# Kernel optimization log

Measured on AMD Instinct MI355X. Metric: run time of the kernel, lower is better.

## Reference

```python
import jax, jax.numpy as jnp
import numpy as np

BN_EPS = 1e-3  # keras BatchNormalization default epsilon


def conv1x1(x, w):
    # x: [N,C,H,W], w: [O,C] (1x1 conv, no bias)
    return jnp.einsum('nchw,oc->nohw', x, w)


def bn(x, gamma, beta, mean, var):
    # inference-mode batchnorm over channel axis 1
    scale = gamma / jnp.sqrt(var + BN_EPS)
    shift = beta - mean * scale
    return x * scale[None, :, None, None] + shift[None, :, None, None]


def fourier_unit(x, w, gamma, beta, mean, var):
    # x: [N,C,H,W] NCHW. 1D rfft over W (matches tf.signal.rfft), normalized by sqrt(W).
    N, C, H, W = x.shape
    norm = jnp.sqrt(jnp.float32(W))
    f = jnp.fft.rfft(x / norm, axis=-1)          # [N,C,H,Wf] complex64, Wf=W//2+1
    Wf = f.shape[-1]
    # interleave re/im per channel: [N,C,2,H,Wf] -> [N,2C,H,Wf]
    ff = jnp.stack([jnp.real(f), jnp.imag(f)], axis=2).reshape(N, 2 * C, H, Wf)
    y = jax.nn.relu(bn(conv1x1(ff, w), gamma, beta, mean, var))  # [N,2C,H,Wf]
    Co = y.shape[1] // 2
    y = y.reshape(N, Co, 2, H, Wf)
    c = jax.lax.complex(y[:, :, 0], y[:, :, 1])
    return jnp.fft.irfft(c, n=W, axis=-1) * norm  # [N,Co,H,W]


def setup_inputs() -> dict:
    key = jax.random.key(0)
    ks = jax.random.split(key, 20)
    N, H, W, Cin = 8, 128, 128, 256
    fmaps = 256
    half = fmaps // 2  # 128

    def nrm(k, shape, s=0.05):
        return jax.random.normal(k, shape, dtype=jnp.float32) * s

    def bn_params(k, c):
        k1, k2, k3, k4 = jax.random.split(k, 4)
        gamma = jax.random.uniform(k1, (c,), dtype=jnp.float32) + 0.5
        beta = nrm(k2, (c,), 0.1)
        mean = nrm(k3, (c,), 0.1)
        var = jax.random.uniform(k4, (c,), dtype=jnp.float32) + 0.5
        return gamma, beta, mean, var

    x = jax.random.normal(ks[0], (N, H, W, Cin), dtype=jnp.float32)
    w1 = nrm(ks[1], (half, Cin))
    g1, b1, m1, v1 = bn_params(ks[2], half)
    fu_w = nrm(ks[3], (2 * half, 2 * half))
    fu_g, fu_b, fu_m, fu_v = bn_params(ks[4], 2 * half)
    lfu_w = nrm(ks[5], (2 * half, 2 * half))
    lfu_g, lfu_b, lfu_m, lfu_v = bn_params(ks[6], 2 * half)
    w2 = nrm(ks[7], (fmaps, half))
    return {
        'x': x, 'w1': w1, 'g1': g1, 'b1': b1, 'm1': m1, 'v1': v1,
        'fu_w': fu_w, 'fu_g': fu_g, 'fu_b': fu_b, 'fu_m': fu_m, 'fu_v': fu_v,
        'lfu_w': lfu_w, 'lfu_g': lfu_g, 'lfu_b': lfu_b, 'lfu_m': lfu_m, 'lfu_v': lfu_v,
        'w2': w2,
    }


def reference(x, w1, g1, b1, m1, v1,
              fu_w, fu_g, fu_b, fu_m, fu_v,
              lfu_w, lfu_g, lfu_b, lfu_m, lfu_v,
              w2):
    # NHWC -> NCHW (stride=1, no downsample)
    x = jnp.transpose(x, (0, 3, 1, 2))
    x = jax.nn.relu(bn(conv1x1(x, w1), g1, b1, m1, v1))  # [N,half,H,W]
    out = fourier_unit(x, fu_w, fu_g, fu_b, fu_m, fu_v)
    # local fourier unit: take first C//4 channels, fold 2x2 spatial patches into channels
    C = x.shape[1]
    xs = x[:, :C // 4]
    xs = jnp.concatenate(jnp.split(xs, 2, axis=2), axis=1)  # split H
    xs = jnp.concatenate(jnp.split(xs, 2, axis=3), axis=1)  # split W -> [N,C,H/2,W/2]
    xs = fourier_unit(xs, lfu_w, lfu_g, lfu_b, lfu_m, lfu_v)
    xs = jnp.tile(xs, (1, 1, 2, 2))  # back to [N,C,H,W]
    out = conv1x1(x + out + xs, w2)  # [N,fmaps,H,W]
    return jnp.transpose(out, (0, 2, 3, 1))  # NCHW -> NHWC
```

## Files before the change

### kernel.cpp

```cpp
#include <hip/hip_runtime.h>
#include <math.h>

typedef __attribute__((ext_vector_type(8))) short short8;
typedef __attribute__((ext_vector_type(4))) float f32x4;

#define SW7b(r) (((r) & 7) << 4)
#define SW3b(r) (((r) & 3) << 4)

static __device__ __forceinline__ unsigned short f2b(float f){
  unsigned u = __float_as_uint(f);
  u = (u + 0x7FFFu + ((u >> 16) & 1u)) >> 16;
  return (unsigned short)u;
}
static __device__ __forceinline__ float b2f(unsigned short u){
  return __uint_as_float(((unsigned)u) << 16);
}
static __device__ __forceinline__ void gl16(const void* g, void* l) {
  __builtin_amdgcn_global_load_lds(
      (const __attribute__((address_space(1))) void*)g,
      (__attribute__((address_space(3))) void*)l, 16, 0, 0);
}

__global__ void k_wt(const float* __restrict__ w1, const float* __restrict__ fu_w,
                     const float* __restrict__ lfu_w, const float* __restrict__ w2,
                     const float* __restrict__ g1, const float* __restrict__ b1,
                     const float* __restrict__ m1, const float* __restrict__ v1,
                     const float* __restrict__ fg, const float* __restrict__ fb,
                     const float* __restrict__ fm, const float* __restrict__ fv,
                     const float* __restrict__ lg_, const float* __restrict__ lb_,
                     const float* __restrict__ lm_, const float* __restrict__ lv_,
                     unsigned short* __restrict__ w1b, unsigned short* __restrict__ fuwb,
                     unsigned short* __restrict__ lfuwb, unsigned short* __restrict__ w2b,
                     unsigned short* __restrict__ DFTf, unsigned short* __restrict__ IDFTf,
                     unsigned short* __restrict__ DFTl, unsigned short* __restrict__ IDFTl,
                     float* __restrict__ sc1, float* __restrict__ sh1,
                     float* __restrict__ scF, float* __restrict__ shF,
                     float* __restrict__ scL, float* __restrict__ shL) {
  int t = blockIdx.x * 256 + threadIdx.x;
  const float TPI = 6.283185307179586f;
  if (t < 32768) {
    { int co = t >> 8, k = t & 255; w1b[co * 256 + (k ^ ((co & 7) << 3))] = f2b(w1[t]); }
    { int co = t >> 7, k = t & 127; w2b[co * 128 + (k ^ ((co & 7) << 3))] = f2b(w2[t]); }
  }
  if (t < 65536) {
    int co = t >> 8, k = t & 255;
    fuwb[co * 256 + (k ^ ((co & 7) << 3))] = f2b(fu_w[t]);
    lfuwb[co * 256 + (k ^ ((co & 7) << 3))] = f2b(lfu_w[t]);
  }
  if (t < 18432) {
    int m = t >> 7, w = t & 127; float v = 0.f;
    if (m < 130) {
      int wf = m >> 1; int ph = (wf * w) & 127;
      float ang = TPI * (float)ph / 128.f;
      v = ((m & 1) ? -sinf(ang) : cosf(ang)) * 0.08838834764831845f;
    }
    DFTf[m * 128 + (w ^ ((m & 7) << 3))] = f2b(v);
  }
  if (t < 24576) {
    int m = t / 192, k2 = t % 192; float v = 0.f;
    if (k2 < 130) {
      int wf = k2 >> 1; float a = (wf == 0 || wf == 64) ? 1.f : 2.f;
      int ph = (wf * m) & 127;
      float ang = TPI * (float)ph / 128.f;
      v = ((k2 & 1) ? -a * sinf(ang) : a * cosf(ang)) * 0.08838834764831845f;
    }
    IDFTf[m * 192 + (k2 ^ ((m & 7) << 3))] = f2b(v);
  }
  if (t < 5120) {
    int m = t >> 6, w = t & 63; float v = 0.f;
    if (m < 66) {
      int wf = m >> 1; int ph = (wf * w) & 63;
      float ang = TPI * (float)ph / 64.f;
      v = ((m & 1) ? -sinf(ang) : cosf(ang)) * 0.125f;
    }
    DFTl[m * 64 + (w ^ ((m & 7) << 3))] = f2b(v);
  }
  if (t < 6144) {
    int m = t / 96, k2 = t % 96; float v = 0.f;
    if (k2 < 66) {
      int wf = k2 >> 1; float a = (wf == 0 || wf == 32) ? 1.f : 2.f;
      int ph = (wf * m) & 63;
      float ang = TPI * (float)ph / 64.f;
      v = ((k2 & 1) ? -a * sinf(ang) : a * cosf(ang)) * 0.125f;
    }
    IDFTl[m * 96 + (k2 ^ ((m & 3) << 3))] = f2b(v);
  }
  if (t < 128) { float s = g1[t] * rsqrtf(v1[t] + 1e-3f); sc1[t] = s; sh1[t] = b1[t] - m1[t] * s; }
  if (t < 256) { float s = fg[t] * rsqrtf(fv[t] + 1e-3f); scF[t] = s; shF[t] = fb[t] - fm[t] * s; }
  if (t < 256) { float s = lg_[t] * rsqrtf(lv_[t] + 1e-3f); scL[t] = s; shL[t] = lb_[t] - lm_[t] * s; }
}

__global__ __launch_bounds__(512) void k_conv1(const unsigned short* __restrict__ A,
                                               const float* __restrict__ x,
                                               unsigned short* __restrict__ X1c,
                                               const float* __restrict__ scp,
                                               const float* __restrict__ shp) {
  __shared__ __align__(16) char A_s[128 * 512];
  __shared__ __align__(16) char B_s[2][32768];
  int t = threadIdx.x; int wid = t >> 6, l = t & 63;
  int wm = wid >> 2, wn = wid & 3;
  int m0 = wm * 64, n0 = wn * 64;
  int lr = l & 15, lg = l >> 4;
  size_t nh0 = (size_t)blockIdx.x * 2;
  const char* Ab = (const char*)A;
  const char* xrow = (const char*)(x + nh0 * 32768);
  #pragma unroll
  for (int i = 0; i < 8; i++) { int g = i * 512 + t; gl16(Ab + g * 16, A_s + g * 16); }
  #pragma unroll
  for (int i = 0; i < 4; i++) {
    int g = i * 512 + t; int w = g >> 3, o = g & 7;
    gl16(xrow + (size_t)w * 1024 + ((o * 16) ^ SW7b(w)), B_s[0] + g * 16);
  }
  f32x4 acc[4][4];
  #pragma unroll
  for (int mt = 0; mt < 4; mt++)
    #pragma unroll
    for (int nt = 0; nt < 4; nt++) acc[mt][nt] = (f32x4){0.f, 0.f, 0.f, 0.f};
  __syncthreads();
  for (int it = 0; it < 8; it++) {
    int kk = it * 32;
    if (it < 7) {
      #pragma unroll
      for (int i = 0; i < 4; i++) {
        int g = i * 512 + t; int w = g >> 3, o = g & 7;
        gl16(xrow + (size_t)w * 1024 + (kk + 32) * 4 + ((o * 16) ^ SW7b(w)),
             B_s[(it + 1) & 1] + g * 16);
      }
    }
    const char* Bc = B_s[it & 1];
    short8 af[4], bf[4];
    #pragma unroll
    for (int mt = 0; mt < 4; mt++) {
      int m = m0 + 16 * mt + lr;
      af[mt] = *(const short8*)(A_s + m * 512 + ((kk * 2 + lg * 16) ^ SW7b(m)));
    }
    #pragma unroll
    for (int nt = 0; nt < 4; nt++) {
      int w = n0 + 16 * nt + lr;
      float4 f0 = *(const float4*)(Bc + w * 128 + ((lg * 32) ^ SW7b(w)));
      float4 f1 = *(const float4*)(Bc + w * 128 + ((lg * 32 + 16) ^ SW7b(w)));
      short8 bb;
      bb[0] = (short)f2b(f0.x); bb[1] = (short)f2b(f0.y);
      bb[2] = (short)f2b(f0.z); bb[3] = (short)f2b(f0.w);
      bb[4] = (short)f2b(f1.x); bb[5] = (short)f2b(f1.y);
      bb[6] = (short)f2b(f1.z); bb[7] = (short)f2b(f1.w);
      bf[nt] = bb;
    }
    #pragma unroll
    for (int mt = 0; mt < 4; mt++)
      #pragma unroll
      for (int nt = 0; nt < 4; nt++)
        acc[mt][nt] = __builtin_amdgcn_mfma_f32_16x16x32_bf16(af[mt], bf[nt], acc[mt][nt], 0, 0, 0);
    __syncthreads();
  }
  #pragma unroll
  for (int nt = 0; nt < 4; nt++) {
    int wcol = n0 + 16 * nt + lr;
    char* xout = (char*)X1c + (nh0 + (wcol >> 7)) * 32768;
    int w = wcol & 127;
    #pragma unroll
    for (int mt = 0; mt < 4; mt++) {
      int rb = m0 + 16 * mt + lg * 4;
      float4 s4 = *(const float4*)&scp[rb];
      float4 h4 = *(const float4*)&shp[rb];
      f32x4 v = acc[mt][nt];
      *(unsigned short*)(xout + (rb + 0) * 256 + ((w * 2) ^ SW7b(rb + 0))) = f2b(fmaxf(v[0] * s4.x + h4.x, 0.f));
      *(unsigned short*)(xout + (rb + 1) * 256 + ((w * 2) ^ SW7b(rb + 1))) = f2b(fmaxf(v[1] * s4.y + h4.y, 0.f));
      *(unsigned short*)(xout + (rb + 2) * 256 + ((w * 2) ^ SW7b(rb + 2))) = f2b(fmaxf(v[2] * s4.z + h4.z, 0.f));
      *(unsigned short*)(xout + (rb + 3) * 256 + ((w * 2) ^ SW7b(rb + 3))) = f2b(fmaxf(v[3] * s4.w + h4.w, 0.f));
    }
  }
}

__global__ __launch_bounds__(256) void k_lfu(const unsigned short* __restrict__ DFTm,
                                             const unsigned short* __restrict__ lfuw,
                                             const unsigned short* __restrict__ IDFTm,
                                             const unsigned short* __restrict__ X1c,
                                             const float* __restrict__ scp,
                                             const float* __restrict__ shp,
                                             unsigned short* __restrict__ XSO) {
  __shared__ __align__(16) char SH[81920];
  char* M   = SH;
  char* Xs  = SH + 16384;
  char* FFl = SH + 32768;
  char* Yl  = SH + 57344;
  int t = threadIdx.x, wid = t >> 6, l = t & 63, lr = l & 15, lg = l >> 4;
  int b = blockIdx.x; int n = b >> 6, h2 = b & 63;
  {
    const char* src = (const char*)DFTm;
    #pragma unroll
    for (int i = 0; i < 3; i++) { int g = i * 256 + t; if (g < 640) gl16(src + g * 16, M + g * 16); }
    #pragma unroll
    for (int i = 0; i < 4; i++) {
      int g = i * 256 + t; int c2 = g >> 3, o = g & 7;
      int c0 = c2 & 31, hb = (c2 >> 5) & 1, wbq = (c2 >> 6) & 1;
      const char* s = (const char*)X1c +
          ((size_t)(n * 128 + hb * 64 + h2) * 128 + c0) * 256 + wbq * 128 + o * 16;
      gl16(s, Xs + g * 16);
    }
    #pragma unroll
    for (int i = 0; i < 8; i++) {
      int u = i * 256 + t;
      if (u < 1920) *(unsigned*)(FFl + 33 * 512 + u * 4) = 0u;
    }
  }
  __syncthreads();
  {
    f32x4 acc[5][2];
    #pragma unroll
    for (int mt = 0; mt < 5; mt++) { acc[mt][0] = (f32x4){0,0,0,0}; acc[mt][1] = (f32x4){0,0,0,0}; }
    for (int kk = 0; kk < 64; kk += 32) {
      int kb = kk * 2 + lg * 16;
      short8 bf[2];
      #pragma unroll
      for (int nt = 0; nt < 2; nt++) {
        int c2 = wid * 32 + 16 * nt + lr;
        bf[nt] = *(const short8*)(Xs + c2 * 128 + (kb ^ SW7b(c2)));
      }
      #pragma unroll
      for (int mt = 0; mt < 5; mt++) {
        int m = 16 * mt + lr;
        short8 af = *(const short8*)(M + m * 128 + (kb ^ SW7b(m)));
        #pragma unroll
        for (int nt = 0; nt < 2; nt++)
          acc[mt][nt] = __builtin_amdgcn_mfma_f32_16x16x32_bf16(af, bf[nt], acc[mt][nt], 0, 0, 0);
      }
    }
    #pragma unroll
    for (int nt = 0; nt < 2; nt++) {
      int c2 = wid * 32 + 16 * nt + lr;
      #pragma unroll
      for (int mt = 0; mt < 5; mt++) {
        int rb = 16 * mt + lg * 4;
        int wf0 = rb >> 1;
        f32x4 v = acc[mt][nt];
        if (wf0 < 33) {
          unsigned pk = (unsigned)f2b(v[0]) | ((unsigned)f2b(v[1]) << 16);
          *(unsigned*)(FFl + wf0 * 512 + ((4 * c2) ^ SW7b(wf0))) = pk;
        }
        if (wf0 + 1 < 33) {
          unsigned pk = (unsigned)f2b(v[2]) | ((unsigned)f2b(v[3]) << 16);
          *(unsigned*)(FFl + (wf0 + 1) * 512 + ((4 * c2) ^ SW7b(wf0 + 1))) = pk;
        }
      }
    }
  }
  __syncthreads();
  int wm2 = wid >> 1, wn2 = wid & 1;
  for (int ch = 0; ch < 8; ch++) {
    {
      const char* src = (const char*)lfuw + (size_t)ch * 16384;
      #pragma unroll
      for (int i = 0; i < 4; i++) { int g = i * 256 + t; gl16(src + g * 16, M + g * 16); }
    }
    __syncthreads();
    int NT = wn2 ? 1 : 2;
    f32x4 acc[2];
    acc[0] = (f32x4){0,0,0,0}; acc[1] = (f32x4){0,0,0,0};
    int lm = wm2 * 16 + lr;
    for (int kk = 0; kk < 256; kk += 32) {
      int kb = kk * 2 + lg * 16;
      short8 af = *(const short8*)(M + lm * 512 + (kb ^ SW7b(lm)));
      #pragma unroll
      for (int j = 0; j < 2; j++) {
        if (j < NT) {
          int wf = wn2 * 32 + 16 * j + lr;
          short8 bf = *(const short8*)(FFl + wf * 512 + (kb ^ SW7b(wf)));
          acc[j] = __builtin_amdgcn_mfma_f32_16x16x32_bf16(af, bf, acc[j], 0, 0, 0);
        }
      }
    }
    int co = ch * 32 + wm2 * 16 + lg * 4;
    float4 s4 = *(const float4*)&scp[co];
    float4 h4 = *(const float4*)&shp[co];
    int cc0 = co >> 1;
    #pragma unroll
    for (int j = 0; j < 2; j++) {
      if (j < NT) {
        int wf = wn2 * 32 + 16 * j + lr;
        f32x4 v = acc[j];
        float v0 = fmaxf(v[0] * s4.x + h4.x, 0.f);
        float v1 = fmaxf(v[1] * s4.y + h4.y, 0.f);
        float v2 = fmaxf(v[2] * s4.z + h4.z, 0.f);
        float v3 = fmaxf(v[3] * s4.w + h4.w, 0.f);
        unsigned p0 = (unsigned)f2b(v0) | ((unsigned)f2b(v1) << 16);
        unsigned p1 = (unsigned)f2b(v2) | ((unsigned)f2b(v3) << 16);
        *(unsigned*)(Yl + (cc0 + 0) * 192 + ((4 * wf) ^ SW3b(cc0 + 0))) = p0;
        *(unsigned*)(Yl + (cc0 + 1) * 192 + ((4 * wf) ^ SW3b(cc0 + 1))) = p1;
      }
    }
    __syncthreads();
  }
  {
    const char* src = (const char*)IDFTm;
    #pragma unroll
    for (int i = 0; i < 3; i++) { int g = i * 256 + t; gl16(src + g * 16, M + g * 16); }
  }
  __syncthreads();
  {
    f32x4 acc[8];
    #pragma unroll
    for (int nt = 0; nt < 8; nt++) acc[nt] = (f32x4){0,0,0,0};
    int w = wid * 16 + lr;
    for (int kk = 0; kk < 96; kk += 32) {
      int kb = kk * 2 + lg * 16;
      short8 af = *(const short8*)(M + w * 192 + (kb ^ SW3b(w)));
      #pragma unroll
      for (int nt = 0; nt < 8; nt++) {
        int cc = 16 * nt + lr;
        short8 bf = *(const short8*)(Yl + cc * 192 + (kb ^ SW3b(cc)));
        acc[nt] = __builtin_amdgcn_mfma_f32_16x16x32_bf16(af, bf, acc[nt], 0, 0, 0);
      }
    }
    int w0 = wid * 16 + lg * 4;
    #pragma unroll
    for (int nt = 0; nt < 8; nt++) {
      int cc = 16 * nt + lr;
      f32x4 v = acc[nt];
      ushort4 o;
      o.x = f2b(v[0]); o.y = f2b(v[1]); o.z = f2b(v[2]); o.w = f2b(v[3]);
      *(ushort4*)(XSO + (((size_t)n * 128 + cc) * 64 + h2) * 64 + w0) = o;
    }
  }
}

__global__ __launch_bounds__(1024, 4) void k_fu(const unsigned short* __restrict__ DFTm,
                                                const unsigned short* __restrict__ fuw,
                                                const unsigned short* __restrict__ IDFTm,
                                                const unsigned short* __restrict__ w2m,
                                                const unsigned short* __restrict__ X1c,
                                                const unsigned short* __restrict__ XSO,
                                                const float* __restrict__ scF,
                                                const float* __restrict__ shF,
                                                float* __restrict__ out) {
  __shared__ __align__(16) char SH[157696];
  char* M0 = SH;
  char* M1 = SH + 36864;
  char* FF = SH + 73728;
  char* Yb = SH + 114688;
  int t = threadIdx.x, wid = t >> 6, l = t & 63, lr = l & 15, lg = l >> 4;
  size_t nh = blockIdx.x;
  int n = (int)(nh >> 7), h = (int)(nh & 127);
  const char* xb = (const char*)X1c + nh * 32768;
  char* Xs = M0 + 0;
  (void)Xs;

  {
    const int nops = 36864 >> 4;
    #pragma unroll
    for (int i_ = 0; i_ < 3; i_++) {
      int g_ = i_ * 1024 + t;
      if (g_ < nops) gl16((const char*)DFTm + (size_t)g_ * 16, M0 + g_ * 16);
    }
    if (t < 1920) *(unsigned*)(FF + 65 * 512 + t * 4) = 0u;
  }
  __syncthreads();
  {
    #pragma unroll
    for (int i_ = 0; i_ < 2; i_++) {
      int g_ = i_ * 1024 + t;
      gl16((const char*)fuw + (size_t)g_ * 16, M1 + g_ * 16);
    }
    int wm1 = wid >> 3, wn1 = wid & 7;
    int c = wn1 * 16 + lr;
    short8 bf[4];
    #pragma unroll
    for (int ks = 0; ks < 4; ks++)
      bf[ks] = *(const short8*)(xb + c * 256 + ((ks * 64 + lg * 16) ^ SW7b(c)));
    f32x4 acc[5];
    #pragma unroll
    for (int mt = 0; mt < 5; mt++) acc[mt] = (f32x4){0,0,0,0};
    #pragma unroll
    for (int ks = 0; ks < 4; ks++) {
      int kb = ks * 64 + lg * 16;
      #pragma unroll
      for (int mt = 0; mt < 5; mt++) {
        int m = 16 * (wm1 * 4 + mt) + lr;
        short8 af = *(const short8*)(M0 + m * 256 + (kb ^ SW7b(m)));
        acc[mt] = __builtin_amdgcn_mfma_f32_16x16x32_bf16(af, bf[ks], acc[mt], 0, 0, 0);
      }
    }
    #pragma unroll
    for (int mt = 0; mt < 5; mt++) {
      int rb = 16 * (wm1 * 4 + mt) + lg * 4;
      int wf0 = rb >> 1;
      f32x4 v = acc[mt];
      if (wf0 < 65) {
        unsigned pk = (unsigned)f2b(v[0]) | ((unsigned)f2b(v[1]) << 16);
        *(unsigned*)(FF + wf0 * 512 + ((4 * c) ^ SW7b(wf0))) = pk;
      }
      if (wf0 + 1 < 65) {
        unsigned pk = (unsigned)f2b(v[2]) | ((unsigned)f2b(v[3]) << 16);
        *(unsigned*)(FF + (wf0 + 1) * 512 + ((4 * c) ^ SW7b(wf0 + 1))) = pk;
      }
    }
  }
  int mb2 = wid & 3, wn2 = wid >> 2;
  int mloc2 = mb2 * 16 + lr;
  #pragma unroll
  for (int ch = 0; ch < 4; ch++) {
    char* Mc = (ch & 1) ? M0 : M1;
    char* Mn = (ch & 1) ? M1 : M0;
    __syncthreads();
    if (ch < 3) {
      #pragma unroll
      for (int i_ = 0; i_ < 2; i_++) {
        int g_ = i_ * 1024 + t;
        gl16((const char*)fuw + (size_t)(ch + 1) * 32768 + (size_t)g_ * 16, Mn + g_ * 16);
      }
    } else {
      #pragma unroll
      for (int i_ = 0; i_ < 2; i_++) {
        int g_ = i_ * 1024 + t;
        if (g_ < 1536) gl16((const char*)IDFTm + (size_t)g_ * 16, Mn + g_ * 16);
      }
    }
    f32x4 acc[2];
    acc[0] = (f32x4){0,0,0,0}; acc[1] = (f32x4){0,0,0,0};
    int NJ = (wn2 == 0) ? 2 : 1;
    int j0 = wn2, j1 = 4;
    #pragma unroll
    for (int ks = 0; ks < 8; ks++) {
      int kb = ks * 64 + lg * 16;
      short8 af = *(const short8*)(Mc + mloc2 * 512 + (kb ^ SW7b(mloc2)));
      {
        int wf = j0 * 16 + lr;
        short8 b0 = *(const short8*)(FF + wf * 512 + (kb ^ SW7b(wf)));
        acc[0] = __builtin_amdgcn_mfma_f32_16x16x32_bf16(af, b0, acc[0], 0, 0, 0);
      }
      if (NJ == 2) {
        int wf = j1 * 16 + lr;
        short8 b1 = *(const short8*)(FF + wf * 512 + (kb ^ SW7b(wf)));
        acc[1] = __builtin_amdgcn_mfma_f32_16x16x32_bf16(af, b1, acc[1], 0, 0, 0);
      }
    }
    int co = ch * 64 + mb2 * 16 + lg * 4;
    float4 s4 = *(const float4*)&scF[co];
    float4 h4 = *(const float4*)&shF[co];
    int cc0 = co >> 1;
    #pragma unroll
    for (int jj = 0; jj < 2; jj++) {
      if (jj < NJ) {
        int wf = (jj == 0 ? j0 : j1) * 16 + lr;
        f32x4 v = acc[jj];
        float v0 = fmaxf(v[0] * s4.x + h4.x, 0.f);
        float v1 = fmaxf(v[1] * s4.y + h4.y, 0.f);
        float v2 = fmaxf(v[2] * s4.z + h4.z, 0.f);
        float v3 = fmaxf(v[3] * s4.w + h4.w, 0.f);
        unsigned p0 = (unsigned)f2b(v0) | ((unsigned)f2b(v1) << 16);
        unsigned p1 = (unsigned)f2b(v2) | ((unsigned)f2b(v3) << 16);
        *(unsigned*)(Yb + (size_t)(cc0 + 0) * 336 + 4 * wf) = p0;
        *(unsigned*)(Yb + (size_t)(cc0 + 1) * 336 + 4 * wf) = p1;
      }
    }
  }
  int mb3 = wid & 3, wn3 = wid >> 2;
  #pragma unroll
  for (int ck = 0; ck < 2; ck++) {
    char* Mc = ck ? M0 : M1;
    __syncthreads();
    if (ck == 0) {
      #pragma unroll
      for (int i_ = 0; i_ < 2; i_++) {
        int g_ = i_ * 1024 + t;
        if (g_ < 1536) gl16((const char*)IDFTm + 24576 + (size_t)g_ * 16, M0 + g_ * 16);
      }
    } else {
      #pragma unroll
      for (int i_ = 0; i_ < 2; i_++) {
        int g_ = i_ * 1024 + t;
        gl16((const char*)w2m + (size_t)g_ * 16, M1 + g_ * 16);
      }
    }
    int mloc = mb3 * 16 + lr;
    int w0 = ck * 64 + mb3 * 16 + lg * 4;
    ushort4 rx[2], rs[2];
    #pragma unroll
    for (int jj = 0; jj < 2; jj++) {
      int cc = (wn3 + jj * 4) * 16 + lr;
      rx[jj] = *(const ushort4*)(xb + cc * 256 + ((w0 * 2) ^ SW7b(cc)));
      rs[jj] = *(const ushort4*)(XSO + (((size_t)n * 128 + cc) * 64 + (h & 63)) * 64 + (w0 & 63));
    }
    f32x4 acc[2];
    acc[0] = (f32x4){0,0,0,0}; acc[1] = (f32x4){0,0,0,0};
    #pragma unroll
    for (int ks = 0; ks < 5; ks++) {
      int kb = ks * 64 + lg * 16;
      short8 af = *(const short8*)(Mc + mloc * 384 + (kb ^ SW7b(mloc)));
      #pragma unroll
      for (int jj = 0; jj < 2; jj++) {
        int cc = (wn3 + jj * 4) * 16 + lr;
        short8 bf = *(const short8*)(Yb + (size_t)cc * 336 + kb);
        acc[jj] = __builtin_amdgcn_mfma_f32_16x16x32_bf16(af, bf, acc[jj], 0, 0, 0);
      }
    }
    #pragma unroll
    for (int jj = 0; jj < 2; jj++) {
      int cc = (wn3 + jj * 4) * 16 + lr;
      f32x4 v = acc[jj];
      float f0 = v[0] + b2f(rx[jj].x) + b2f(rs[jj].x);
      float f1 = v[1] + b2f(rx[jj].y) + b2f(rs[jj].y);
      float f2_ = v[2] + b2f(rx[jj].z) + b2f(rs[jj].z);
      float f3 = v[3] + b2f(rx[jj].w) + b2f(rs[jj].w);
      *(unsigned short*)(FF + (w0 + 0) * 256 + ((cc * 2) ^ SW7b(w0 + 0))) = f2b(f0);
      *(unsigned short*)(FF + (w0 + 1) * 256 + ((cc * 2) ^ SW7b(w0 + 1))) = f2b(f1);
      *(unsigned short*)(FF + (w0 + 2) * 256 + ((cc * 2) ^ SW7b(w0 + 2))) = f2b(f2_);
      *(unsigned short*)(FF + (w0 + 3) * 256 + ((cc * 2) ^ SW7b(w0 + 3))) = f2b(f3);
    }
  }
  int mb4 = wid & 7, wn4 = wid >> 3;
  int mloc4 = mb4 * 16 + lr;
  #pragma unroll
  for (int ck = 0; ck < 2; ck++) {
    char* Mc = ck ? M0 : M1;
    __syncthreads();
    if (ck == 0) {
      #pragma unroll
      for (int i_ = 0; i_ < 2; i_++) {
        int g_ = i_ * 1024 + t;
        gl16((const char*)w2m + 32768 + (size_t)g_ * 16, M0 + g_ * 16);
      }
    }
    f32x4 acc[4];
    #pragma unroll
    for (int nt = 0; nt < 4; nt++) acc[nt] = (f32x4){0,0,0,0};
    #pragma unroll
    for (int ks = 0; ks < 4; ks++) {
      int kb = ks * 64 + lg * 16;
      short8 af = *(const short8*)(Mc + mloc4 * 256 + (kb ^ SW7b(mloc4)));
      #pragma unroll
      for (int nt = 0; nt < 4; nt++) {
        int w = (wn4 * 4 + nt) * 16 + lr;
        short8 bf = *(const short8*)(FF + w * 256 + (kb ^ SW7b(w)));
        acc[nt] = __builtin_amdgcn_mfma_f32_16x16x32_bf16(af, bf, acc[nt], 0, 0, 0);
      }
    }
    int co2 = ck * 128 + mb4 * 16 + lg * 4;
    #pragma unroll
    for (int nt = 0; nt < 4; nt++) {
      int w = (wn4 * 4 + nt) * 16 + lr;
      f32x4 v = acc[nt];
      float4 o; o.x = v[0]; o.y = v[1]; o.z = v[2]; o.w = v[3];
      *(float4*)(out + (nh * 128 + w) * 256 + co2) = o;
    }
  }
}

extern "C" void kernel_launch(void* const* d_in, const int* in_sizes, int n_in,
                              void* d_out, int out_size, void* d_ws, size_t ws_size,
                              hipStream_t stream) {
  const float* x     = (const float*)d_in[0];
  const float* w1    = (const float*)d_in[1];
  const float* g1    = (const float*)d_in[2];
  const float* b1    = (const float*)d_in[3];
  const float* m1    = (const float*)d_in[4];
  const float* v1    = (const float*)d_in[5];
  const float* fu_w  = (const float*)d_in[6];
  const float* fu_g  = (const float*)d_in[7];
  const float* fu_b  = (const float*)d_in[8];
  const float* fu_m  = (const float*)d_in[9];
  const float* fu_v  = (const float*)d_in[10];
  const float* lfu_w = (const float*)d_in[11];
  const float* lfu_g = (const float*)d_in[12];
  const float* lfu_b = (const float*)d_in[13];
  const float* lfu_m = (const float*)d_in[14];
  const float* lfu_v = (const float*)d_in[15];
  const float* w2    = (const float*)d_in[16];
  float* out = (float*)d_out;

  char* p = (char*)d_ws;
  unsigned short* X1c = (unsigned short*)p; p += 33554432;
  unsigned short* XSO = (unsigned short*)p; p += 8388608;
  unsigned short* w1b   = (unsigned short*)p; p += 65536;
  unsigned short* fuwb  = (unsigned short*)p; p += 131072;
  unsigned short* lfuwb = (unsigned short*)p; p += 131072;
  unsigned short* w2b   = (unsigned short*)p; p += 65536;
  unsigned short* DFTf  = (unsigned short*)p; p += 36864;
  unsigned short* IDFTf = (unsigned short*)p; p += 49152;
  unsigned short* DFTl  = (unsigned short*)p; p += 10240;
  unsigned short* IDFTl = (unsigned short*)p; p += 12288;
  float* sc1 = (float*)p; p += 512;
  float* sh1 = (float*)p; p += 512;
  float* scF = (float*)p; p += 1024;
  float* shF = (float*)p; p += 1024;
  float* scL = (float*)p; p += 1024;
  float* shL = (float*)p; p += 1024;

  k_wt<<<dim3(256), dim3(256), 0, stream>>>(w1, fu_w, lfu_w, w2, g1, b1, m1, v1,
                                            fu_g, fu_b, fu_m, fu_v, lfu_g, lfu_b, lfu_m, lfu_v,
                                            w1b, fuwb, lfuwb, w2b, DFTf, IDFTf, DFTl, IDFTl,
                                            sc1, sh1, scF, shF, scL, shL);
  k_conv1<<<dim3(512), dim3(512), 0, stream>>>(w1b, x, X1c, sc1, sh1);
  k_lfu<<<dim3(512), dim3(256), 0, stream>>>(DFTl, lfuwb, IDFTl, X1c, scL, shL, XSO);
  k_fu<<<dim3(1024), dim3(1024), 0, stream>>>(DFTf, fuwb, IDFTf, w2b, X1c, XSO, scF, shF, out);
}
```

Baseline: 152.3 us.

## Rewrite k_fu stages with 32x32x16 MFMA tiles and wider LDS swizzles

The fused Fourier-unit kernel moves from 16x16x32 MFMA tiles to 32x32x16 tiles in all four GEMM stages (DFT, spectral 1x1 conv, inverse DFT, output conv). Weight and DFT matrix layouts change to a 16-row XOR swizzle and a K-chunked fu_w layout to match, and the DFT table is padded. The inverse DFT now runs as a single pass over all 128 outputs instead of two chunks, which removes barriers. The intent is fewer LDS fragment loads per MFMA and fewer synchronisation points, at the cost of more accumulator registers and a slightly larger LDS footprint.

```diff
diff --git a/kernel.cpp b/kernel.cpp
--- a/kernel.cpp
+++ b/kernel.cpp
@@ -3,9 +3,12 @@
 
 typedef __attribute__((ext_vector_type(8))) short short8;
 typedef __attribute__((ext_vector_type(4))) float f32x4;
+typedef __attribute__((ext_vector_type(16))) float f32x16;
 
 #define SW7b(r) (((r) & 7) << 4)
 #define SW3b(r) (((r) & 3) << 4)
+#define K15(r) (((r) & 15) << 4)
+#define K7(r)  (((r) & 7) << 4)
 
 static __device__ __forceinline__ unsigned short f2b(float f){
   unsigned u = __float_as_uint(f);
@@ -40,21 +43,21 @@
   const float TPI = 6.283185307179586f;
   if (t < 32768) {
     { int co = t >> 8, k = t & 255; w1b[co * 256 + (k ^ ((co & 7) << 3))] = f2b(w1[t]); }
-    { int co = t >> 7, k = t & 127; w2b[co * 128 + (k ^ ((co & 7) << 3))] = f2b(w2[t]); }
+    { int co = t >> 7, k = t & 127; w2b[co * 128 + (k ^ ((co & 15) << 3))] = f2b(w2[t]); }
   }
   if (t < 65536) {
     int co = t >> 8, k = t & 255;
-    fuwb[co * 256 + (k ^ ((co & 7) << 3))] = f2b(fu_w[t]);
+    fuwb[(size_t)(k >> 6) * 16384 + co * 64 + ((k & 63) ^ ((co & 7) << 3))] = f2b(fu_w[t]);
     lfuwb[co * 256 + (k ^ ((co & 7) << 3))] = f2b(lfu_w[t]);
   }
-  if (t < 18432) {
+  if (t < 20480) {
     int m = t >> 7, w = t & 127; float v = 0.f;
     if (m < 130) {
       int wf = m >> 1; int ph = (wf * w) & 127;
       float ang = TPI * (float)ph / 128.f;
       v = ((m & 1) ? -sinf(ang) : cosf(ang)) * 0.08838834764831845f;
     }
-    DFTf[m * 128 + (w ^ ((m & 7) << 3))] = f2b(v);
+    DFTf[m * 128 + (w ^ ((m & 15) << 3))] = f2b(v);
   }
   if (t < 24576) {
     int m = t / 192, k2 = t % 192; float v = 0.f;
@@ -164,10 +167,10 @@
       float4 s4 = *(const float4*)&scp[rb];
       float4 h4 = *(const float4*)&shp[rb];
       f32x4 v = acc[mt][nt];
-      *(unsigned short*)(xout + (rb + 0) * 256 + ((w * 2) ^ SW7b(rb + 0))) = f2b(fmaxf(v[0] * s4.x + h4.x, 0.f));
-      *(unsigned short*)(xout + (rb + 1) * 256 + ((w * 2) ^ SW7b(rb + 1))) = f2b(fmaxf(v[1] * s4.y + h4.y, 0.f));
-      *(unsigned short*)(xout + (rb + 2) * 256 + ((w * 2) ^ SW7b(rb + 2))) = f2b(fmaxf(v[2] * s4.z + h4.z, 0.f));
-      *(unsigned short*)(xout + (rb + 3) * 256 + ((w * 2) ^ SW7b(rb + 3))) = f2b(fmaxf(v[3] * s4.w + h4.w, 0.f));
+      *(unsigned short*)(xout + (rb + 0) * 256 + ((w * 2) ^ K15(rb + 0))) = f2b(fmaxf(v[0] * s4.x + h4.x, 0.f));
+      *(unsigned short*)(xout + (rb + 1) * 256 + ((w * 2) ^ K15(rb + 1))) = f2b(fmaxf(v[1] * s4.y + h4.y, 0.f));
+      *(unsigned short*)(xout + (rb + 2) * 256 + ((w * 2) ^ K15(rb + 2))) = f2b(fmaxf(v[2] * s4.z + h4.z, 0.f));
+      *(unsigned short*)(xout + (rb + 3) * 256 + ((w * 2) ^ K15(rb + 3))) = f2b(fmaxf(v[3] * s4.w + h4.w, 0.f));
     }
   }
 }
@@ -194,8 +197,9 @@
     for (int i = 0; i < 4; i++) {
       int g = i * 256 + t; int c2 = g >> 3, o = g & 7;
       int c0 = c2 & 31, hb = (c2 >> 5) & 1, wbq = (c2 >> 6) & 1;
+      int half = wbq ^ ((c0 >> 3) & 1);
       const char* s = (const char*)X1c +
-          ((size_t)(n * 128 + hb * 64 + h2) * 128 + c0) * 256 + wbq * 128 + o * 16;
+          ((size_t)(n * 128 + hb * 64 + h2) * 128 + c0) * 256 + half * 128 + o * 16;
       gl16(s, Xs + g * 16);
     }
     #pragma unroll
@@ -333,215 +337,206 @@
                                                 const float* __restrict__ scF,
                                                 const float* __restrict__ shF,
                                                 float* __restrict__ out) {
-  __shared__ __align__(16) char SH[157696];
-  char* M0 = SH;
-  char* M1 = SH + 36864;
-  char* FF = SH + 73728;
-  char* Yb = SH + 114688;
-  int t = threadIdx.x, wid = t >> 6, l = t & 63, lr = l & 15, lg = l >> 4;
+  __shared__ __align__(16) char SH[161792];
+  char* R0 = SH;
+  char* R1 = SH + 40960;
+  char* R2 = SH + 73728;
+  char* R3 = SH + 122880;
+  int t = threadIdx.x, wid = t >> 6, l = t & 63;
+  int lc = l & 31, hf = l >> 5;
   size_t nh = blockIdx.x;
-  int n = (int)(nh >> 7), h = (int)(nh & 127);
+  int n = (int)(nh >> 7), hh = (int)(nh & 127);
   const char* xb = (const char*)X1c + nh * 32768;
-  char* Xs = M0 + 0;
-  (void)Xs;
-
-  {
-    const int nops = 36864 >> 4;
-    #pragma unroll
-    for (int i_ = 0; i_ < 3; i_++) {
-      int g_ = i_ * 1024 + t;
-      if (g_ < nops) gl16((const char*)DFTm + (size_t)g_ * 16, M0 + g_ * 16);
-    }
-    if (t < 1920) *(unsigned*)(FF + 65 * 512 + t * 4) = 0u;
-  }
-  __syncthreads();
-  {
-    #pragma unroll
-    for (int i_ = 0; i_ < 2; i_++) {
-      int g_ = i_ * 1024 + t;
-      gl16((const char*)fuw + (size_t)g_ * 16, M1 + g_ * 16);
-    }
-    int wm1 = wid >> 3, wn1 = wid & 7;
-    int c = wn1 * 16 + lr;
-    short8 bf[4];
-    #pragma unroll
-    for (int ks = 0; ks < 4; ks++)
-      bf[ks] = *(const short8*)(xb + c * 256 + ((ks * 64 + lg * 16) ^ SW7b(c)));
-    f32x4 acc[5];
-    #pragma unroll
-    for (int mt = 0; mt < 5; mt++) acc[mt] = (f32x4){0,0,0,0};
-    #pragma unroll
-    for (int ks = 0; ks < 4; ks++) {
-      int kb = ks * 64 + lg * 16;
-      #pragma unroll
-      for (int mt = 0; mt < 5; mt++) {
-        int m = 16 * (wm1 * 4 + mt) + lr;
-        short8 af = *(const short8*)(M0 + m * 256 + (kb ^ SW7b(m)));
-        acc[mt] = __builtin_amdgcn_mfma_f32_16x16x32_bf16(af, bf[ks], acc[mt], 0, 0, 0);
-      }
-    }
-    #pragma unroll
-    for (int mt = 0; mt < 5; mt++) {
-      int rb = 16 * (wm1 * 4 + mt) + lg * 4;
-      int wf0 = rb >> 1;
-      f32x4 v = acc[mt];
-      if (wf0 < 65) {
-        unsigned pk = (unsigned)f2b(v[0]) | ((unsigned)f2b(v[1]) << 16);
-        *(unsigned*)(FF + wf0 * 512 + ((4 * c) ^ SW7b(wf0))) = pk;
-      }
-      if (wf0 + 1 < 65) {
-        unsigned pk = (unsigned)f2b(v[2]) | ((unsigned)f2b(v[3]) << 16);
-        *(unsigned*)(FF + (wf0 + 1) * 512 + ((4 * c) ^ SW7b(wf0 + 1))) = pk;
-      }
-    }
-  }
-  int mb2 = wid & 3, wn2 = wid >> 2;
-  int mloc2 = mb2 * 16 + lr;
-  #pragma unroll
-  for (int ch = 0; ch < 4; ch++) {
-    char* Mc = (ch & 1) ? M0 : M1;
-    char* Mn = (ch & 1) ? M1 : M0;
-    __syncthreads();
-    if (ch < 3) {
-      #pragma unroll
-      for (int i_ = 0; i_ < 2; i_++) {
-        int g_ = i_ * 1024 + t;
-        gl16((const char*)fuw + (size_t)(ch + 1) * 32768 + (size_t)g_ * 16, Mn + g_ * 16);
-      }
-    } else {
-      #pragma unroll
-      for (int i_ = 0; i_ < 2; i_++) {
-        int g_ = i_ * 1024 + t;
-        if (g_ < 1536) gl16((const char*)IDFTm + (size_t)g_ * 16, Mn + g_ * 16);
-      }
-    }
-    f32x4 acc[2];
-    acc[0] = (f32x4){0,0,0,0}; acc[1] = (f32x4){0,0,0,0};
-    int NJ = (wn2 == 0) ? 2 : 1;
-    int j0 = wn2, j1 = 4;
+
+  #pragma unroll
+  for (int i = 0; i < 3; i++) {
+    int g = i * 1024 + t;
+    if (g < 2560) gl16((const char*)DFTm + (size_t)g * 16, R0 + g * 16);
+  }
+  *(unsigned*)(R2 + 80 * 512 + t * 8) = 0u;
+  *(unsigned*)(R2 + 80 * 512 + t * 8 + 4) = 0u;
+  __syncthreads();
+  {
+    #pragma unroll
+    for (int i = 0; i < 2; i++) {
+      int g = i * 1024 + t;
+      gl16((const char*)fuw + (size_t)g * 16, R1 + g * 16);
+    }
+    int mb = wid & 3, nb = wid >> 2;
+    int c = nb * 32 + lc;
+    short8 bfp[8];
+    #pragma unroll
+    for (int ks = 0; ks < 8; ks++)
+      bfp[ks] = *(const short8*)(xb + (size_t)c * 256 + ((ks * 32 + hf * 16) ^ K15(c)));
+    f32x16 acc0 = {0}, acc1 = {0};
+    bool x2 = (wid < 4);
+    int c2b = wid * 32 + lc;
     #pragma unroll
     for (int ks = 0; ks < 8; ks++) {
-      int kb = ks * 64 + lg * 16;
-      short8 af = *(const short8*)(Mc + mloc2 * 512 + (kb ^ SW7b(mloc2)));
+      int ko = ks * 32 + hf * 16;
+      int m = mb * 32 + lc;
+      short8 af = *(const short8*)(R0 + (size_t)m * 256 + (ko ^ K15(m)));
+      acc0 = __builtin_amdgcn_mfma_f32_32x32x16_bf16(af, bfp[ks], acc0, 0, 0, 0);
+      if (x2) {
+        int m2 = 128 + lc;
+        short8 af2 = *(const short8*)(R0 + (size_t)m2 * 256 + (ko ^ K15(m2)));
+        short8 bf2 = *(const short8*)(xb + (size_t)c2b * 256 + (ko ^ K15(c2b)));
+        acc1 = __builtin_amdgcn_mfma_f32_32x32x16_bf16(af2, bf2, acc1, 0, 0, 0);
+      }
+    }
+    #pragma unroll
+    for (int q = 0; q < 4; q++) {
+      int wfe = mb * 16 + 4 * q + 2 * hf;
+      unsigned p0 = (unsigned)f2b(acc0[4 * q + 0]) | ((unsigned)f2b(acc0[4 * q + 1]) << 16);
+      unsigned p1 = (unsigned)f2b(acc0[4 * q + 2]) | ((unsigned)f2b(acc0[4 * q + 3]) << 16);
+      *(unsigned*)(R2 + (size_t)wfe * 512 + ((4 * c) ^ K15(wfe))) = p0;
+      *(unsigned*)(R2 + (size_t)(wfe + 1) * 512 + ((4 * c) ^ K15(wfe + 1))) = p1;
+    }
+    if (x2) {
+      #pragma unroll
+      for (int q = 0; q < 4; q++) {
+        int wfe = 64 + 4 * q + 2 * hf;
+        unsigned p0 = (unsigned)f2b(acc1[4 * q + 0]) | ((unsigned)f2b(acc1[4 * q + 1]) << 16);
+        unsigned p1 = (unsigned)f2b(acc1[4 * q + 2]) | ((unsigned)f2b(acc1[4 * q + 3]) << 16);
+        *(unsigned*)(R2 + (size_t)wfe * 512 + ((4 * c2b) ^ K15(wfe))) = p0;
+        *(unsigned*)(R2 + (size_t)(wfe + 1) * 512 + ((4 * c2b) ^ K15(wfe + 1))) = p1;
+      }
+    }
+  }
+  {
+    int mb = wid >> 1, odd = wid & 1;
+    int co = mb * 32 + lc;
+    f32x16 pa = {0}, pb = {0};
+    int wfA = (odd ? 32 : 0) + lc;
+    int wfB = 64 + lc;
+    #pragma unroll
+    for (int ch = 0; ch < 4; ch++) {
+      char* Mc = (ch & 1) ? R0 : R1;
+      char* Mn = (ch & 1) ? R1 : R0;
+      __syncthreads();
+      if (ch < 3) {
+        #pragma unroll
+        for (int i = 0; i < 2; i++) {
+          int g = i * 1024 + t;
+          gl16((const char*)fuw + (size_t)(ch + 1) * 32768 + (size_t)g * 16, Mn + g * 16);
+        }
+      } else {
+        #pragma unroll
+        for (int i = 0; i < 2; i++) {
+          int g = i * 1024 + t;
+          gl16((const char*)w2m + (size_t)g * 16, Mn + g * 16);
+        }
+      }
+      #pragma unroll
+      for (int ks = 0; ks < 4; ks++) {
+        int ko = ks * 32 + hf * 16;
+        short8 af = *(const short8*)(Mc + (size_t)co * 128 + (ko ^ K7(co)));
+        int kg = (ch * 4 + ks) * 32 + hf * 16;
+        short8 bfA = *(const short8*)(R2 + (size_t)wfA * 512 + (kg ^ K15(wfA)));
+        pa = __builtin_amdgcn_mfma_f32_32x32x16_bf16(af, bfA, pa, 0, 0, 0);
+        if (!odd) {
+          short8 bfB = *(const short8*)(R2 + (size_t)wfB * 512 + (kg ^ K15(wfB)));
+          pb = __builtin_amdgcn_mfma_f32_32x32x16_bf16(af, bfB, pb, 0, 0, 0);
+        }
+      }
+    }
+    #pragma unroll
+    for (int q = 0; q < 4; q++) {
+      int co0 = mb * 32 + 8 * q + 4 * hf;
+      float4 s4 = *(const float4*)&scF[co0];
+      float4 h4 = *(const float4*)&shF[co0];
+      int cc0 = co0 >> 1;
       {
-        int wf = j0 * 16 + lr;
-        short8 b0 = *(const short8*)(FF + wf * 512 + (kb ^ SW7b(wf)));
-        acc[0] = __builtin_amdgcn_mfma_f32_16x16x32_bf16(af, b0, acc[0], 0, 0, 0);
-      }
-      if (NJ == 2) {
-        int wf = j1 * 16 + lr;
-        short8 b1 = *(const short8*)(FF + wf * 512 + (kb ^ SW7b(wf)));
-        acc[1] = __builtin_amdgcn_mfma_f32_16x16x32_bf16(af, b1, acc[1], 0, 0, 0);
-      }
-    }
-    int co = ch * 64 + mb2 * 16 + lg * 4;
-    float4 s4 = *(const float4*)&scF[co];
-    float4 h4 = *(const float4*)&shF[co];
-    int cc0 = co >> 1;
-    #pragma unroll
-    for (int jj = 0; jj < 2; jj++) {
-      if (jj < NJ) {
-        int wf = (jj == 0 ? j0 : j1) * 16 + lr;
-        f32x4 v = acc[jj];
-        float v0 = fmaxf(v[0] * s4.x + h4.x, 0.f);
-        float v1 = fmaxf(v[1] * s4.y + h4.y, 0.f);
-        float v2 = fmaxf(v[2] * s4.z + h4.z, 0.f);
-        float v3 = fmaxf(v[3] * s4.w + h4.w, 0.f);
+        float v0 = fmaxf(pa[4 * q + 0] * s4.x + h4.x, 0.f);
+        float v1 = fmaxf(pa[4 * q + 1] * s4.y + h4.y, 0.f);
+        float v2 = fmaxf(pa[4 * q + 2] * s4.z + h4.z, 0.f);
+        float v3 = fmaxf(pa[4 * q + 3] * s4.w + h4.w, 0.f);
         unsigned p0 = (unsigned)f2b(v0) | ((unsigned)f2b(v1) << 16);
         unsigned p1 = (unsigned)f2b(v2) | ((unsigned)f2b(v3) << 16);
-        *(unsigned*)(Yb + (size_t)(cc0 + 0) * 336 + 4 * wf) = p0;
-        *(unsigned*)(Yb + (size_t)(cc0 + 1) * 336 + 4 * wf) = p1;
-      }
-    }
-  }
-  int mb3 = wid & 3, wn3 = wid >> 2;
-  #pragma unroll
-  for (int ck = 0; ck < 2; ck++) {
-    char* Mc = ck ? M0 : M1;
+        *(unsigned*)(R3 + (size_t)(cc0 + 0) * 304 + 4 * wfA) = p0;
+        *(unsigned*)(R3 + (size_t)(cc0 + 1) * 304 + 4 * wfA) = p1;
+      }
+      if (!odd && lc < 12) {
+        float v0 = fmaxf(pb[4 * q + 0] * s4.x + h4.x, 0.f);
+        float v1 = fmaxf(pb[4 * q + 1] * s4.y + h4.y, 0.f);
+        float v2 = fmaxf(pb[4 * q + 2] * s4.z + h4.z, 0.f);
+        float v3 = fmaxf(pb[4 * q + 3] * s4.w + h4.w, 0.f);
+        unsigned p0 = (unsigned)f2b(v0) | ((unsigned)f2b(v1) << 16);
+        unsigned p1 = (unsigned)f2b(v2) | ((unsigned)f2b(v3) << 16);
+        *(unsigned*)(R3 + (size_t)(cc0 + 0) * 304 + 4 * wfB) = p0;
+        *(unsigned*)(R3 + (size_t)(cc0 + 1) * 304 + 4 * wfB) = p1;
+      }
+    }
+  }
+  __syncthreads();
+  #pragma unroll
+  for (int i = 0; i < 3; i++) {
+    int g = i * 1024 + t;
+    gl16((const char*)IDFTm + (size_t)g * 16, R2 + g * 16);
+  }
+  #pragma unroll
+  for (int i = 0; i < 2; i++) {
+    int g = i * 1024 + t;
+    gl16((const char*)w2m + 32768 + (size_t)g * 16, R0 + g * 16);
+  }
+  __syncthreads();
+  {
+    int mb = wid & 3, nb = wid >> 2;
+    int mw = mb * 32 + lc;
+    int cc = nb * 32 + lc;
+    f32x16 p3 = {0};
+    #pragma unroll
+    for (int ks = 0; ks < 9; ks++) {
+      int ko = ks * 32 + hf * 16;
+      short8 af = *(const short8*)(R2 + (size_t)mw * 384 + (ko ^ K7(mw)));
+      short8 bf = *(const short8*)(R3 + (size_t)cc * 304 + ko);
+      p3 = __builtin_amdgcn_mfma_f32_32x32x16_bf16(af, bf, p3, 0, 0, 0);
+    }
+    ushort4 rx[4], rs[4];
+    #pragma unroll
+    for (int q = 0; q < 4; q++) {
+      int w0 = mb * 32 + 8 * q + 4 * hf;
+      rx[q] = *(const ushort4*)(xb + (size_t)cc * 256 + ((2 * w0) ^ K15(cc)));
+      rs[q] = *(const ushort4*)(XSO + (((size_t)n * 128 + cc) * 64 + (hh & 63)) * 64 + (w0 & 63));
+    }
     __syncthreads();
-    if (ck == 0) {
-      #pragma unroll
-      for (int i_ = 0; i_ < 2; i_++) {
-        int g_ = i_ * 1024 + t;
-        if (g_ < 1536) gl16((const char*)IDFTm + 24576 + (size_t)g_ * 16, M0 + g_ * 16);
-      }
-    } else {
-      #pragma unroll
-      for (int i_ = 0; i_ < 2; i_++) {
-        int g_ = i_ * 1024 + t;
-        gl16((const char*)w2m + (size_t)g_ * 16, M1 + g_ * 16);
-      }
-    }
-    int mloc = mb3 * 16 + lr;
-    int w0 = ck * 64 + mb3 * 16 + lg * 4;
-    ushort4 rx[2], rs[2];
-    #pragma unroll
-    for (int jj = 0; jj < 2; jj++) {
-      int cc = (wn3 + jj * 4) * 16 + lr;
-      rx[jj] = *(const ushort4*)(xb + cc * 256 + ((w0 * 2) ^ SW7b(cc)));
-      rs[jj] = *(const ushort4*)(XSO + (((size_t)n * 128 + cc) * 64 + (h & 63)) * 64 + (w0 & 63));
-    }
-    f32x4 acc[2];
-    acc[0] = (f32x4){0,0,0,0}; acc[1] = (f32x4){0,0,0,0};
-    #pragma unroll
-    for (int ks = 0; ks < 5; ks++) {
-      int kb = ks * 64 + lg * 16;
-      short8 af = *(const short8*)(Mc + mloc * 384 + (kb ^ SW7b(mloc)));
-      #pragma unroll
-      for (int jj = 0; jj < 2; jj++) {
-        int cc = (wn3 + jj * 4) * 16 + lr;
-        short8 bf = *(const short8*)(Yb + (size_t)cc * 336 + kb);
-        acc[jj] = __builtin_amdgcn_mfma_f32_16x16x32_bf16(af, bf, acc[jj], 0, 0, 0);
-      }
-    }
-    #pragma unroll
-    for (int jj = 0; jj < 2; jj++) {
-      int cc = (wn3 + jj * 4) * 16 + lr;
-      f32x4 v = acc[jj];
-      float f0 = v[0] + b2f(rx[jj].x) + b2f(rs[jj].x);
-      float f1 = v[1] + b2f(rx[jj].y) + b2f(rs[jj].y);
-      float f2_ = v[2] + b2f(rx[jj].z) + b2f(rs[jj].z);
-      float f3 = v[3] + b2f(rx[jj].w) + b2f(rs[jj].w);
-      *(unsigned short*)(FF + (w0 + 0) * 256 + ((cc * 2) ^ SW7b(w0 + 0))) = f2b(f0);
-      *(unsigned short*)(FF + (w0 + 1) * 256 + ((cc * 2) ^ SW7b(w0 + 1))) = f2b(f1);
-      *(unsigned short*)(FF + (w0 + 2) * 256 + ((cc * 2) ^ SW7b(w0 + 2))) = f2b(f2_);
-      *(unsigned short*)(FF + (w0 + 3) * 256 + ((cc * 2) ^ SW7b(w0 + 3))) = f2b(f3);
-    }
-  }
-  int mb4 = wid & 7, wn4 = wid >> 3;
-  int mloc4 = mb4 * 16 + lr;
-  #pragma unroll
-  for (int ck = 0; ck < 2; ck++) {
-    char* Mc = ck ? M0 : M1;
-    __syncthreads();
-    if (ck == 0) {
-      #pragma unroll
-      for (int i_ = 0; i_ < 2; i_++) {
-        int g_ = i_ * 1024 + t;
-        gl16((const char*)w2m + 32768 + (size_t)g_ * 16, M0 + g_ * 16);
-      }
-    }
-    f32x4 acc[4];
-    #pragma unroll
-    for (int nt = 0; nt < 4; nt++) acc[nt] = (f32x4){0,0,0,0};
-    #pragma unroll
-    for (int ks = 0; ks < 4; ks++) {
-      int kb = ks * 64 + lg * 16;
-      short8 af = *(const short8*)(Mc + mloc4 * 256 + (kb ^ SW7b(mloc4)));
-      #pragma unroll
-      for (int nt = 0; nt < 4; nt++) {
-        int w = (wn4 * 4 + nt) * 16 + lr;
-        short8 bf = *(const short8*)(FF + w * 256 + (kb ^ SW7b(w)));
-        acc[nt] = __builtin_amdgcn_mfma_f32_16x16x32_bf16(af, bf, acc[nt], 0, 0, 0);
-      }
-    }
-    int co2 = ck * 128 + mb4 * 16 + lg * 4;
-    #pragma unroll
-    for (int nt = 0; nt < 4; nt++) {
-      int w = (wn4 * 4 + nt) * 16 + lr;
-      f32x4 v = acc[nt];
-      float4 o; o.x = v[0]; o.y = v[1]; o.z = v[2]; o.w = v[3];
-      *(float4*)(out + (nh * 128 + w) * 256 + co2) = o;
+    #pragma unroll
+    for (int q = 0; q < 4; q++) {
+      int w0 = mb * 32 + 8 * q + 4 * hf;
+      float f0 = p3[4 * q + 0] + b2f(rx[q].x) + b2f(rs[q].x);
+      float f1 = p3[4 * q + 1] + b2f(rx[q].y) + b2f(rs[q].y);
+      float f2_ = p3[4 * q + 2] + b2f(rx[q].z) + b2f(rs[q].z);
+      float f3 = p3[4 * q + 3] + b2f(rx[q].w) + b2f(rs[q].w);
+      *(unsigned short*)(R3 + (size_t)(w0 + 0) * 256 + ((2 * cc) ^ K15(w0 + 0))) = f2b(f0);
+      *(unsigned short*)(R3 + (size_t)(w0 + 1) * 256 + ((2 * cc) ^ K15(w0 + 1))) = f2b(f1);
+      *(unsigned short*)(R3 + (size_t)(w0 + 2) * 256 + ((2 * cc) ^ K15(w0 + 2))) = f2b(f2_);
+      *(unsigned short*)(R3 + (size_t)(w0 + 3) * 256 + ((2 * cc) ^ K15(w0 + 3))) = f2b(f3);
+    }
+  }
+  __syncthreads();
+  {
+    int mb = wid & 3, nb = wid >> 2;
+    int mco = mb * 32 + lc;
+    int nw = nb * 32 + lc;
+    #pragma unroll
+    for (int ck = 0; ck < 2; ck++) {
+      const char* Mc = ck ? R0 : R1;
+      f32x16 p4 = {0};
+      #pragma unroll
+      for (int ks = 0; ks < 8; ks++) {
+        int ko = ks * 32 + hf * 16;
+        short8 af = *(const short8*)(Mc + (size_t)mco * 256 + (ko ^ K15(mco)));
+        short8 bf = *(const short8*)(R3 + (size_t)nw * 256 + (ko ^ K15(nw)));
+        p4 = __builtin_amdgcn_mfma_f32_32x32x16_bf16(af, bf, p4, 0, 0, 0);
+      }
+      #pragma unroll
+      for (int q = 0; q < 4; q++) {
+        int co2 = ck * 128 + mb * 32 + 8 * q + 4 * hf;
+        float4 o;
+        o.x = p4[4 * q + 0]; o.y = p4[4 * q + 1];
+        o.z = p4[4 * q + 2]; o.w = p4[4 * q + 3];
+        *(float4*)(out + (nh * 128 + nw) * 256 + co2) = o;
+      }
     }
   }
 }
@@ -575,7 +570,7 @@
   unsigned short* fuwb  = (unsigned short*)p; p += 131072;
   unsigned short* lfuwb = (unsigned short*)p; p += 131072;
   unsigned short* w2b   = (unsigned short*)p; p += 65536;
-  unsigned short* DFTf  = (unsigned short*)p; p += 36864;
+  unsigned short* DFTf  = (unsigned short*)p; p += 40960;
   unsigned short* IDFTf = (unsigned short*)p; p += 49152;
   unsigned short* DFTl  = (unsigned short*)p; p += 10240;
   unsigned short* IDFTl = (unsigned short*)p; p += 12288;
```

Measured after the change: 148.0 us. 2.8% less time.
